# Kernel tuning notes

Measured on AMD Instinct MI355X. Metric: run time of the kernel, lower is better.

Reference implementation:

```python
import jax, jax.numpy as jnp
import numpy as np

N_NODES = 100000
N_EDGES = 1600000
IN_DIM = 256
HIDDEN = 64


def setup_inputs() -> dict:
    key = jax.random.key(0)
    k0, k1, k2, k3 = jax.random.split(key, 4)
    x = jax.random.normal(k0, (N_NODES, IN_DIM), dtype=jnp.float32)
    edge_index = jax.random.randint(k1, (2, N_EDGES), 0, N_NODES, dtype=jnp.int64)
    # GCNConv weight [in_dim, hidden] + bias, MLP Linear(hidden, 1) + bias
    W = jax.random.normal(k2, (IN_DIM, HIDDEN), dtype=jnp.float32) * 0.05
    b = jnp.zeros((HIDDEN,), dtype=jnp.float32)
    w2 = jax.random.normal(k3, (HIDDEN, 1), dtype=jnp.float32) * 0.05
    b2 = jnp.zeros((1,), dtype=jnp.float32)
    return {"x": x, "edge_index": edge_index, "W": W, "b": b, "w2": w2, "b2": b2}


def reference(x, edge_index, W, b, w2, b2):
    N = x.shape[0]
    # PyG GCNConv default: add self-loops, symmetric normalization D^-1/2 A D^-1/2
    loops = jnp.arange(N, dtype=edge_index.dtype)
    src = jnp.concatenate([edge_index[0], loops])  # [E + N]
    dst = jnp.concatenate([edge_index[1], loops])
    h = x @ W  # [N, H] transform first (hidden < in_dim)
    deg = jax.ops.segment_sum(jnp.ones_like(dst, dtype=h.dtype), dst, num_segments=N)
    dinv = jnp.where(deg > 0, jax.lax.rsqrt(deg), 0.0)
    norm = dinv[src] * dinv[dst]  # [E + N]
    agg = jax.ops.segment_sum(h[src] * norm[:, None], dst, num_segments=N) + b  # [N, H]
    score = jax.nn.sigmoid(agg @ w2 + b2)  # [N, 1]
    return score.squeeze(-1)
```

## Files before the change

kernel.cpp:

```cpp
#include <hip/hip_runtime.h>
#include <math.h>

#define N_NODES 100000
#define N_EDGES 1600000
#define IN_DIM  256
#define HIDDEN  64

#define NB      32
#define EPB     50000
#define QPB     12500
#define SR      8
#define SRANGE  12544
#define PD      8
#define DNR     12800
#define DW      3200

__global__ void wv_kernel(const float* __restrict__ W, const float* __restrict__ b,
                          const float* __restrict__ w2, const float* __restrict__ b2,
                          float* __restrict__ v, float* __restrict__ c) {
    int i = threadIdx.x;
    float acc = 0.f;
    #pragma unroll 8
    for (int j = 0; j < HIDDEN; ++j) acc += W[i * HIDDEN + j] * w2[j];
    v[i] = acc;
    if (i == 0) {
        float cc = b2[0];
        for (int j = 0; j < HIDDEN; ++j) cc += b[j] * w2[j];
        *c = cc;
    }
}

__global__ void s_kernel(const float* __restrict__ x, const float* __restrict__ v,
                         float* __restrict__ s) {
    const int wave = threadIdx.x >> 6;
    const int lane = threadIdx.x & 63;
    const int n = blockIdx.x * 4 + wave;
    const float4* xr = (const float4*)(x + (size_t)n * IN_DIM);
    const float4* vr = (const float4*)v;
    float4 a  = xr[lane];
    float4 vv = vr[lane];
    float d = a.x * vv.x + a.y * vv.y + a.z * vv.z + a.w * vv.w;
    #pragma unroll
    for (int off = 32; off > 0; off >>= 1) d += __shfl_down(d, off, 64);
    if (lane == 0) s[n] = d;
}

__global__ void __launch_bounds__(512) deg_hist_kernel(const int4* __restrict__ dst4,
                                                       unsigned* __restrict__ partialD) {
    __shared__ unsigned hist[DW];
    const int r  = blockIdx.x & (PD - 1);
    const int bb = blockIdx.x >> 3;
    const int nbase = r * DNR;
    for (int i = threadIdx.x; i < DW; i += 512) hist[i] = 0u;
    __syncthreads();
    const int q0 = bb * QPB;
    for (int k = threadIdx.x; k < QPB; k += 512) {
        int4 d4 = dst4[q0 + k];
        int d0 = d4.x - nbase, d1 = d4.y - nbase, d2 = d4.z - nbase, d3 = d4.w - nbase;
        if ((unsigned)d0 < (unsigned)DNR) atomicAdd(&hist[d0 >> 2], 1u << ((d0 & 3) * 8));
        if ((unsigned)d1 < (unsigned)DNR) atomicAdd(&hist[d1 >> 2], 1u << ((d1 & 3) * 8));
        if ((unsigned)d2 < (unsigned)DNR) atomicAdd(&hist[d2 >> 2], 1u << ((d2 & 3) * 8));
        if ((unsigned)d3 < (unsigned)DNR) atomicAdd(&hist[d3 >> 2], 1u << ((d3 & 3) * 8));
    }
    __syncthreads();
    unsigned* outp = partialD + (size_t)blockIdx.x * DW;
    for (int i = threadIdx.x; i < DW; i += 512) outp[i] = hist[i];
}

__global__ void deg_merge_kernel(const unsigned* __restrict__ partialD,
                                 const float* __restrict__ s,
                                 float* __restrict__ dinv, float* __restrict__ t) {
    int w = blockIdx.x * blockDim.x + threadIdx.x;
    if (w >= N_NODES / 4) return;
    const int r = w / DW, j = w - r * DW;
    unsigned a0 = 0, a1 = 0, a2 = 0, a3 = 0;
    #pragma unroll 8
    for (int b = 0; b < NB; ++b) {
        unsigned p = partialD[(size_t)(b * PD + r) * DW + j];
        a0 += p & 255u; a1 += (p >> 8) & 255u; a2 += (p >> 16) & 255u; a3 += p >> 24;
    }
    const int n0 = w * 4;
    float4 sv = *(const float4*)(s + n0);
    float4 di, tv;
    di.x = rsqrtf((float)(a0 + 1)); di.y = rsqrtf((float)(a1 + 1));
    di.z = rsqrtf((float)(a2 + 1)); di.w = rsqrtf((float)(a3 + 1));
    tv.x = di.x * sv.x; tv.y = di.y * sv.y; tv.z = di.z * sv.z; tv.w = di.w * sv.w;
    *(float4*)(dinv + n0) = di;
    *(float4*)(t + n0) = tv;
}

__global__ void __launch_bounds__(512) scat_hist_kernel(const int4* __restrict__ src4,
                                                        const int4* __restrict__ dst4,
                                                        const float* __restrict__ t,
                                                        float* __restrict__ partialU) {
    __shared__ float acc[SRANGE];
    const int r  = blockIdx.x & (SR - 1);
    const int bb = blockIdx.x >> 3;
    const int nbase = r * SRANGE;
    for (int i = threadIdx.x; i < SRANGE; i += 512) acc[i] = 0.f;
    __syncthreads();
    const int q0 = bb * QPB;
    for (int k = threadIdx.x; k < QPB; k += 512) {
        int4 d4 = dst4[q0 + k];
        int4 s4 = src4[q0 + k];
        int d0 = d4.x - nbase, d1 = d4.y - nbase, d2 = d4.z - nbase, d3 = d4.w - nbase;
        if ((unsigned)d0 < (unsigned)SRANGE) atomicAdd(&acc[d0], t[s4.x]);
        if ((unsigned)d1 < (unsigned)SRANGE) atomicAdd(&acc[d1], t[s4.y]);
        if ((unsigned)d2 < (unsigned)SRANGE) atomicAdd(&acc[d2], t[s4.z]);
        if ((unsigned)d3 < (unsigned)SRANGE) atomicAdd(&acc[d3], t[s4.w]);
    }
    __syncthreads();
    float* outp = partialU + (size_t)blockIdx.x * SRANGE;
    for (int i = threadIdx.x; i < SRANGE; i += 512) outp[i] = acc[i];
}

__global__ void merge_final_kernel(const float* __restrict__ partialU,
                                   const float* __restrict__ dinv,
                                   const float* __restrict__ s,
                                   const float* __restrict__ c,
                                   float* __restrict__ out) {
    int n = blockIdx.x * blockDim.x + threadIdx.x;
    if (n >= N_NODES) return;
    const int r = n / SRANGE, j = n - r * SRANGE;
    float u = 0.f;
    #pragma unroll 8
    for (int b = 0; b < NB; ++b)
        u += partialU[(size_t)(b * SR + r) * SRANGE + j];
    float di = dinv[n];
    float pre = di * (u + di * s[n]) + c[0];
    out[n] = 1.f / (1.f + expf(-pre));
}

__global__ void deg_kernel(const int* __restrict__ dst, int* __restrict__ cnt) {
    int e = blockIdx.x * blockDim.x + threadIdx.x;
    if (e < N_EDGES) atomicAdd(&cnt[dst[e]], 1);
}
__global__ void dinv_kernel(const int* __restrict__ cnt, const float* __restrict__ s,
                            float* __restrict__ dinv, float* __restrict__ t) {
    int n = blockIdx.x * blockDim.x + threadIdx.x;
    if (n < N_NODES) {
        float di = rsqrtf((float)(cnt[n] + 1));
        dinv[n] = di;
        t[n] = di * s[n];
    }
}
__global__ void scatter_kernel(const int* __restrict__ src, const int* __restrict__ dst,
                               const float* __restrict__ t, float* __restrict__ u) {
    int e = blockIdx.x * blockDim.x + threadIdx.x;
    if (e < N_EDGES) atomicAdd(&u[dst[e]], t[src[e]]);
}
__global__ void final_kernel(const float* __restrict__ dinv, const float* __restrict__ u,
                             const float* __restrict__ s, const float* __restrict__ c,
                             float* __restrict__ out) {
    int n = blockIdx.x * blockDim.x + threadIdx.x;
    if (n < N_NODES) {
        float di = dinv[n];
        float pre = di * (u[n] + di * s[n]) + c[0];
        out[n] = 1.f / (1.f + expf(-pre));
    }
}

extern "C" void kernel_launch(void* const* d_in, const int* in_sizes, int n_in,
                              void* d_out, int out_size, void* d_ws, size_t ws_size,
                              hipStream_t stream) {
    const float* x   = (const float*)d_in[0];
    const int*   ei  = (const int*)  d_in[1];
    const float* W   = (const float*)d_in[2];
    const float* b   = (const float*)d_in[3];
    const float* w2  = (const float*)d_in[4];
    const float* b2  = (const float*)d_in[5];
    float* out = (float*)d_out;

    const int* src = ei;
    const int* dst = ei + N_EDGES;

    float* ws   = (float*)d_ws;
    float*    v        = ws + 0;
    float*    c        = ws + 256;
    float*    s        = ws + 512;
    float*    t        = ws + 100608;
    float*    dinv     = ws + 200704;
    unsigned* partialD = (unsigned*)(ws + 300800);
    float*    partialU = ws + 1120000;
    const size_t need_bytes = (size_t)(1120000 + NB * SR * SRANGE) * 4;

    wv_kernel<<<1, 256, 0, stream>>>(W, b, w2, b2, v, c);
    s_kernel<<<N_NODES / 4, 256, 0, stream>>>(x, v, s);

    if (ws_size >= need_bytes) {
        deg_hist_kernel<<<NB * PD, 512, 0, stream>>>((const int4*)dst, partialD);
        deg_merge_kernel<<<(N_NODES / 4 + 255) / 256, 256, 0, stream>>>(partialD, s, dinv, t);
        scat_hist_kernel<<<NB * SR, 512, 0, stream>>>((const int4*)src, (const int4*)dst, t, partialU);
        merge_final_kernel<<<(N_NODES + 511) / 512, 512, 0, stream>>>(partialU, dinv, s, c, out);
    } else {
        float* u   = ws + 300800;
        int*   cnt = (int*)(ws + 400800);
        hipMemsetAsync((char*)d_ws + (size_t)300800 * 4, 0, (size_t)200000 * 4, stream);
        deg_kernel<<<(N_EDGES + 255) / 256, 256, 0, stream>>>(dst, cnt);
        dinv_kernel<<<(N_NODES + 255) / 256, 256, 0, stream>>>(cnt, s, dinv, t);
        scatter_kernel<<<(N_EDGES + 255) / 256, 256, 0, stream>>>(src, dst, t, u);
        final_kernel<<<(N_NODES + 255) / 256, 256, 0, stream>>>(dinv, u, s, c, out);
    }
}
```

Before: 223.4 us.

## Fuse weight-vector, node projection and degree histogram into one heterogeneous kernel

Merges wv_kernel, s_kernel and deg_hist_kernel into one launch. The first 256 blocks build the degree histograms, and the remaining 256 blocks each recompute v=W·w2 in shared memory and grid-stride over nodes to compute s. The bias constant c is now recomputed per thread in merge_final, which removes the separate wv launch. Scatter blocks are widened to 1024 threads. The aim is fewer launches and overlap of the x-streaming dot products with the edge histogram; the cost is redundant v computation in every block and more LDS atomic contention per block.

```diff
diff --git a/kernel.cpp b/kernel.cpp
--- a/kernel.cpp
+++ b/kernel.cpp
@@ -14,13 +14,137 @@
 #define PD      8
 #define DNR     12800
 #define DW      3200
+#define DEGB    256
+
+__global__ void __launch_bounds__(1024) fusedA_kernel(const float* __restrict__ x,
+                                                      const float* __restrict__ W,
+                                                      const float* __restrict__ w2,
+                                                      const int4* __restrict__ dst4,
+                                                      unsigned* __restrict__ partialD,
+                                                      float* __restrict__ s) {
+    __shared__ __align__(16) unsigned sh[DW];
+    const int bid = blockIdx.x;
+    if (bid < DEGB) {
+        const int r  = bid & (PD - 1);
+        const int bb = bid >> 3;
+        const int nbase = r * DNR;
+        for (int i = threadIdx.x; i < DW; i += 1024) sh[i] = 0u;
+        __syncthreads();
+        const int q0 = bb * QPB;
+        for (int k = threadIdx.x; k < QPB; k += 1024) {
+            int4 d4 = dst4[q0 + k];
+            int d0 = d4.x - nbase, d1 = d4.y - nbase, d2 = d4.z - nbase, d3 = d4.w - nbase;
+            if ((unsigned)d0 < (unsigned)DNR) atomicAdd(&sh[d0 >> 2], 1u << ((d0 & 3) * 8));
+            if ((unsigned)d1 < (unsigned)DNR) atomicAdd(&sh[d1 >> 2], 1u << ((d1 & 3) * 8));
+            if ((unsigned)d2 < (unsigned)DNR) atomicAdd(&sh[d2 >> 2], 1u << ((d2 & 3) * 8));
+            if ((unsigned)d3 < (unsigned)DNR) atomicAdd(&sh[d3 >> 2], 1u << ((d3 & 3) * 8));
+        }
+        __syncthreads();
+        unsigned* outp = partialD + (size_t)bid * DW;
+        for (int i = threadIdx.x; i < DW; i += 1024) outp[i] = sh[i];
+    } else {
+        float* vsh = (float*)sh;
+        if (threadIdx.x < IN_DIM) {
+            const float4* wr  = (const float4*)(W + threadIdx.x * HIDDEN);
+            const float4* w2r = (const float4*)w2;
+            float acc = 0.f;
+            #pragma unroll
+            for (int j = 0; j < HIDDEN / 4; ++j) {
+                float4 a = wr[j], q = w2r[j];
+                acc += a.x * q.x + a.y * q.y + a.z * q.z + a.w * q.w;
+            }
+            vsh[threadIdx.x] = acc;
+        }
+        __syncthreads();
+        const int wid  = threadIdx.x >> 6;
+        const int lane = threadIdx.x & 63;
+        const int gw   = (bid - DEGB) * 16 + wid;
+        float4 vv = ((const float4*)vsh)[lane];
+        for (int n = gw; n < N_NODES; n += 4096) {
+            const float4* xr = (const float4*)(x + (size_t)n * IN_DIM);
+            float4 a = xr[lane];
+            float d = a.x * vv.x + a.y * vv.y + a.z * vv.z + a.w * vv.w;
+            #pragma unroll
+            for (int off = 32; off > 0; off >>= 1) d += __shfl_down(d, off, 64);
+            if (lane == 0) s[n] = d;
+        }
+    }
+}
+
+__global__ void deg_merge_kernel(const unsigned* __restrict__ partialD,
+                                 const float* __restrict__ s,
+                                 float* __restrict__ dinv, float* __restrict__ t) {
+    int w = blockIdx.x * blockDim.x + threadIdx.x;
+    if (w >= N_NODES / 4) return;
+    const int r = w / DW, j = w - r * DW;
+    unsigned a0 = 0, a1 = 0, a2 = 0, a3 = 0;
+    #pragma unroll 8
+    for (int b = 0; b < NB; ++b) {
+        unsigned p = partialD[(size_t)(b * PD + r) * DW + j];
+        a0 += p & 255u; a1 += (p >> 8) & 255u; a2 += (p >> 16) & 255u; a3 += p >> 24;
+    }
+    const int n0 = w * 4;
+    float4 sv = *(const float4*)(s + n0);
+    float4 di, tv;
+    di.x = rsqrtf((float)(a0 + 1)); di.y = rsqrtf((float)(a1 + 1));
+    di.z = rsqrtf((float)(a2 + 1)); di.w = rsqrtf((float)(a3 + 1));
+    tv.x = di.x * sv.x; tv.y = di.y * sv.y; tv.z = di.z * sv.z; tv.w = di.w * sv.w;
+    *(float4*)(dinv + n0) = di;
+    *(float4*)(t + n0) = tv;
+}
+
+__global__ void __launch_bounds__(1024) scat_hist_kernel(const int4* __restrict__ src4,
+                                                         const int4* __restrict__ dst4,
+                                                         const float* __restrict__ t,
+                                                         float* __restrict__ partialU) {
+    __shared__ float acc[SRANGE];
+    const int r  = blockIdx.x & (SR - 1);
+    const int bb = blockIdx.x >> 3;
+    const int nbase = r * SRANGE;
+    for (int i = threadIdx.x; i < SRANGE; i += 1024) acc[i] = 0.f;
+    __syncthreads();
+    const int q0 = bb * QPB;
+    for (int k = threadIdx.x; k < QPB; k += 1024) {
+        int4 d4 = dst4[q0 + k];
+        int4 s4 = src4[q0 + k];
+        int d0 = d4.x - nbase, d1 = d4.y - nbase, d2 = d4.z - nbase, d3 = d4.w - nbase;
+        if ((unsigned)d0 < (unsigned)SRANGE) atomicAdd(&acc[d0], t[s4.x]);
+        if ((unsigned)d1 < (unsigned)SRANGE) atomicAdd(&acc[d1], t[s4.y]);
+        if ((unsigned)d2 < (unsigned)SRANGE) atomicAdd(&acc[d2], t[s4.z]);
+        if ((unsigned)d3 < (unsigned)SRANGE) atomicAdd(&acc[d3], t[s4.w]);
+    }
+    __syncthreads();
+    float* outp = partialU + (size_t)blockIdx.x * SRANGE;
+    for (int i = threadIdx.x; i < SRANGE; i += 1024) outp[i] = acc[i];
+}
+
+__global__ void merge_final_kernel(const float* __restrict__ partialU,
+                                   const float* __restrict__ dinv,
+                                   const float* __restrict__ s,
+                                   const float* __restrict__ b,
+                                   const float* __restrict__ w2,
+                                   const float* __restrict__ b2,
+                                   float* __restrict__ out) {
+    float c = b2[0];
+    #pragma unroll 8
+    for (int j = 0; j < HIDDEN; ++j) c += b[j] * w2[j];
+    int n = blockIdx.x * blockDim.x + threadIdx.x;
+    if (n >= N_NODES) return;
+    const int r = n / SRANGE, j = n - r * SRANGE;
+    float u = 0.f;
+    #pragma unroll 8
+    for (int bl = 0; bl < NB; ++bl)
+        u += partialU[(size_t)(bl * SR + r) * SRANGE + j];
+    float di = dinv[n];
+    float pre = di * (u + di * s[n]) + c;
+    out[n] = 1.f / (1.f + expf(-pre));
+}
 
 __global__ void wv_kernel(const float* __restrict__ W, const float* __restrict__ b,
                           const float* __restrict__ w2, const float* __restrict__ b2,
                           float* __restrict__ v, float* __restrict__ c) {
     int i = threadIdx.x;
     float acc = 0.f;
-    #pragma unroll 8
     for (int j = 0; j < HIDDEN; ++j) acc += W[i * HIDDEN + j] * w2[j];
     v[i] = acc;
     if (i == 0) {
@@ -29,7 +153,6 @@
         *c = cc;
     }
 }
-
 __global__ void s_kernel(const float* __restrict__ x, const float* __restrict__ v,
                          float* __restrict__ s) {
     const int wave = threadIdx.x >> 6;
@@ -44,93 +167,6 @@
     for (int off = 32; off > 0; off >>= 1) d += __shfl_down(d, off, 64);
     if (lane == 0) s[n] = d;
 }
-
-__global__ void __launch_bounds__(512) deg_hist_kernel(const int4* __restrict__ dst4,
-                                                       unsigned* __restrict__ partialD) {
-    __shared__ unsigned hist[DW];
-    const int r  = blockIdx.x & (PD - 1);
-    const int bb = blockIdx.x >> 3;
-    const int nbase = r * DNR;
-    for (int i = threadIdx.x; i < DW; i += 512) hist[i] = 0u;
-    __syncthreads();
-    const int q0 = bb * QPB;
-    for (int k = threadIdx.x; k < QPB; k += 512) {
-        int4 d4 = dst4[q0 + k];
-        int d0 = d4.x - nbase, d1 = d4.y - nbase, d2 = d4.z - nbase, d3 = d4.w - nbase;
-        if ((unsigned)d0 < (unsigned)DNR) atomicAdd(&hist[d0 >> 2], 1u << ((d0 & 3) * 8));
-        if ((unsigned)d1 < (unsigned)DNR) atomicAdd(&hist[d1 >> 2], 1u << ((d1 & 3) * 8));
-        if ((unsigned)d2 < (unsigned)DNR) atomicAdd(&hist[d2 >> 2], 1u << ((d2 & 3) * 8));
-        if ((unsigned)d3 < (unsigned)DNR) atomicAdd(&hist[d3 >> 2], 1u << ((d3 & 3) * 8));
-    }
-    __syncthreads();
-    unsigned* outp = partialD + (size_t)blockIdx.x * DW;
-    for (int i = threadIdx.x; i < DW; i += 512) outp[i] = hist[i];
-}
-
-__global__ void deg_merge_kernel(const unsigned* __restrict__ partialD,
-                                 const float* __restrict__ s,
-                                 float* __restrict__ dinv, float* __restrict__ t) {
-    int w = blockIdx.x * blockDim.x + threadIdx.x;
-    if (w >= N_NODES / 4) return;
-    const int r = w / DW, j = w - r * DW;
-    unsigned a0 = 0, a1 = 0, a2 = 0, a3 = 0;
-    #pragma unroll 8
-    for (int b = 0; b < NB; ++b) {
-        unsigned p = partialD[(size_t)(b * PD + r) * DW + j];
-        a0 += p & 255u; a1 += (p >> 8) & 255u; a2 += (p >> 16) & 255u; a3 += p >> 24;
-    }
-    const int n0 = w * 4;
-    float4 sv = *(const float4*)(s + n0);
-    float4 di, tv;
-    di.x = rsqrtf((float)(a0 + 1)); di.y = rsqrtf((float)(a1 + 1));
-    di.z = rsqrtf((float)(a2 + 1)); di.w = rsqrtf((float)(a3 + 1));
-    tv.x = di.x * sv.x; tv.y = di.y * sv.y; tv.z = di.z * sv.z; tv.w = di.w * sv.w;
-    *(float4*)(dinv + n0) = di;
-    *(float4*)(t + n0) = tv;
-}
-
-__global__ void __launch_bounds__(512) scat_hist_kernel(const int4* __restrict__ src4,
-                                                        const int4* __restrict__ dst4,
-                                                        const float* __restrict__ t,
-                                                        float* __restrict__ partialU) {
-    __shared__ float acc[SRANGE];
-    const int r  = blockIdx.x & (SR - 1);
-    const int bb = blockIdx.x >> 3;
-    const int nbase = r * SRANGE;
-    for (int i = threadIdx.x; i < SRANGE; i += 512) acc[i] = 0.f;
-    __syncthreads();
-    const int q0 = bb * QPB;
-    for (int k = threadIdx.x; k < QPB; k += 512) {
-        int4 d4 = dst4[q0 + k];
-        int4 s4 = src4[q0 + k];
-        int d0 = d4.x - nbase, d1 = d4.y - nbase, d2 = d4.z - nbase, d3 = d4.w - nbase;
-        if ((unsigned)d0 < (unsigned)SRANGE) atomicAdd(&acc[d0], t[s4.x]);
-        if ((unsigned)d1 < (unsigned)SRANGE) atomicAdd(&acc[d1], t[s4.y]);
-        if ((unsigned)d2 < (unsigned)SRANGE) atomicAdd(&acc[d2], t[s4.z]);
-        if ((unsigned)d3 < (unsigned)SRANGE) atomicAdd(&acc[d3], t[s4.w]);
-    }
-    __syncthreads();
-    float* outp = partialU + (size_t)blockIdx.x * SRANGE;
-    for (int i = threadIdx.x; i < SRANGE; i += 512) outp[i] = acc[i];
-}
-
-__global__ void merge_final_kernel(const float* __restrict__ partialU,
-                                   const float* __restrict__ dinv,
-                                   const float* __restrict__ s,
-                                   const float* __restrict__ c,
-                                   float* __restrict__ out) {
-    int n = blockIdx.x * blockDim.x + threadIdx.x;
-    if (n >= N_NODES) return;
-    const int r = n / SRANGE, j = n - r * SRANGE;
-    float u = 0.f;
-    #pragma unroll 8
-    for (int b = 0; b < NB; ++b)
-        u += partialU[(size_t)(b * SR + r) * SRANGE + j];
-    float di = dinv[n];
-    float pre = di * (u + di * s[n]) + c[0];
-    out[n] = 1.f / (1.f + expf(-pre));
-}
-
 __global__ void deg_kernel(const int* __restrict__ dst, int* __restrict__ cnt) {
     int e = blockIdx.x * blockDim.x + threadIdx.x;
     if (e < N_EDGES) atomicAdd(&cnt[dst[e]], 1);
@@ -182,20 +218,19 @@
     float*    dinv     = ws + 200704;
     unsigned* partialD = (unsigned*)(ws + 300800);
     float*    partialU = ws + 1120000;
-    const size_t need_bytes = (size_t)(1120000 + NB * SR * SRANGE) * 4;
-
-    wv_kernel<<<1, 256, 0, stream>>>(W, b, w2, b2, v, c);
-    s_kernel<<<N_NODES / 4, 256, 0, stream>>>(x, v, s);
+    const size_t need_bytes = (size_t)(1120000 + 256 * SRANGE) * 4;
 
     if (ws_size >= need_bytes) {
-        deg_hist_kernel<<<NB * PD, 512, 0, stream>>>((const int4*)dst, partialD);
+        fusedA_kernel<<<DEGB + 256, 1024, 0, stream>>>(x, W, w2, (const int4*)dst, partialD, s);
         deg_merge_kernel<<<(N_NODES / 4 + 255) / 256, 256, 0, stream>>>(partialD, s, dinv, t);
-        scat_hist_kernel<<<NB * SR, 512, 0, stream>>>((const int4*)src, (const int4*)dst, t, partialU);
-        merge_final_kernel<<<(N_NODES + 511) / 512, 512, 0, stream>>>(partialU, dinv, s, c, out);
+        scat_hist_kernel<<<NB * SR, 1024, 0, stream>>>((const int4*)src, (const int4*)dst, t, partialU);
+        merge_final_kernel<<<(N_NODES + 511) / 512, 512, 0, stream>>>(partialU, dinv, s, b, w2, b2, out);
     } else {
         float* u   = ws + 300800;
         int*   cnt = (int*)(ws + 400800);
         hipMemsetAsync((char*)d_ws + (size_t)300800 * 4, 0, (size_t)200000 * 4, stream);
+        wv_kernel<<<1, 256, 0, stream>>>(W, b, w2, b2, v, c);
+        s_kernel<<<N_NODES / 4, 256, 0, stream>>>(x, v, s);
         deg_kernel<<<(N_EDGES + 255) / 256, 256, 0, stream>>>(dst, cnt);
         dinv_kernel<<<(N_NODES + 255) / 256, 256, 0, stream>>>(cnt, s, dinv, t);
         scatter_kernel<<<(N_EDGES + 255) / 256, 256, 0, stream>>>(src, dst, t, u);
```

After: 207.2 us. 7.3% less time.
